# Kernel tuning notes

Measured on AMD Instinct MI355X. Metric: run time of the kernel, lower is better.

Reference implementation:

```python
import jax, jax.numpy as jnp
import numpy as np

N = 20000       # nodes per graph
E = 320000      # edges per graph (avg degree 16)
R = 8           # num_relations
B = 2           # batch of graphs
DIMS = [128, 256, 256, 128]  # in -> hidden -> hidden -> out
SLOPE = 0.2     # LeakyReLU negative slope


def setup_inputs() -> dict:
    key = jax.random.key(0)
    ks = jax.random.split(key, 12)
    inp = {
        "x": jax.random.normal(ks[0], (B, N, DIMS[0]), dtype=jnp.float32),
        "edge_index": jax.random.randint(ks[1], (B, 2, E), 0, N, dtype=jnp.int32),
        "edge_type": jax.random.randint(ks[2], (B, E), 0, R, dtype=jnp.int32),
    }
    for l in range(3):
        cin, cout = DIMS[l], DIMS[l + 1]
        s = 1.0 / np.sqrt(cin)
        inp[f"W{l}"] = jax.random.normal(ks[3 + 3 * l], (R, cin, cout), jnp.float32) * s
        inp[f"root{l}"] = jax.random.normal(ks[4 + 3 * l], (cin, cout), jnp.float32) * s
        inp[f"b{l}"] = jnp.zeros((cout,), jnp.float32)
    return inp


def _rgcn_layer(h, src, dst, etype, W, root, b):
    """One RGCNConv (per-relation mean aggregation) on a single graph.
    h: (N,Cin), src/dst/etype: (E,), W: (R,Cin,Cout), root: (Cin,Cout), b: (Cout,)
    """
    # transform every node by every relation weight once: (N,R,Cout)
    h_rel = jnp.einsum('nc,rcd->nrd', h, W)
    # per-edge message: gather source node transformed by that edge's relation
    msg = h_rel[src, etype]                               # (E,Cout)
    # per-(target-node, relation) mean, as in PyG's per-relation propagate
    seg = dst * R + etype                                 # (E,)
    sums = jax.ops.segment_sum(msg, seg, num_segments=N * R)
    cnt = jax.ops.segment_sum(jnp.ones((msg.shape[0],), h.dtype), seg,
                              num_segments=N * R)
    mean = sums / jnp.maximum(cnt, 1.0)[:, None]          # (N*R,Cout)
    agg = mean.reshape(N, R, -1).sum(axis=1)              # (N,Cout)
    return agg + h @ root + b


def reference(x, edge_index, edge_type, W0, root0, b0, W1, root1, b1, W2, root2, b2):
    params = [(W0, root0, b0), (W1, root1, b1), (W2, root2, b2)]

    def single(xg, ei, et):
        src, dst = ei[0], ei[1]
        h = xg
        for (W, root, b) in params:
            h = _rgcn_layer(h, src, dst, et, W, root, b)
            h = jnp.where(h > 0, h, SLOPE * h)  # LeakyReLU(0.2); dropout=identity (eval)
        return h

    return jax.vmap(single)(x, edge_index, edge_type)
```

## Files before the change

kernel.cpp:

```cpp
#include <hip/hip_runtime.h>
#include <hip/hip_bf16.h>

#define NN 20000
#define EE 320000
#define RR 8
#define NR (NN * RR)
#define NB 40
#define SCAP 640

typedef float f32x4 __attribute__((ext_vector_type(4)));
typedef float f32x2 __attribute__((ext_vector_type(2)));
typedef short s16x8 __attribute__((ext_vector_type(8)));

__device__ __forceinline__ unsigned short f2bf(float f) {
  unsigned u = __builtin_bit_cast(unsigned, f);
  unsigned r = u + 0x7FFFu + ((u >> 16) & 1u);
  return (unsigned short)(r >> 16);
}
__device__ __forceinline__ f32x2 bf2x2(unsigned u) {
  f32x2 r;
  r.x = __builtin_bit_cast(float, u << 16);
  r.y = __builtin_bit_cast(float, u & 0xFFFF0000u);
  return r;
}
__device__ __forceinline__ void gload_lds16(const void* g, void* l) {
  __builtin_amdgcn_global_load_lds(
      (const __attribute__((address_space(1))) unsigned*)g,
      (__attribute__((address_space(3))) unsigned*)l, 16, 0, 0);
}

__global__ void k_count(const int* __restrict__ ei, const int* __restrict__ et,
                        int* __restrict__ cnt) {
  int e = blockIdx.x * blockDim.x + threadIdx.x;
  int g = e >= EE;
  int el = e - g * EE;
  int d = ei[(size_t)g * 2 * EE + EE + el];
  int t = et[(size_t)g * EE + el];
  atomicAdd(&cnt[(size_t)g * NR + d * RR + t], 1);
}

__global__ __launch_bounds__(1024) void k_scan1(const int* __restrict__ cnt,
                                                int* __restrict__ off,
                                                int* __restrict__ btot) {
  int g = blockIdx.y, b = blockIdx.x;
  const int* c = cnt + (size_t)g * NR;
  int* o = off + (size_t)g * NR;
  __shared__ int wsum[16];
  int lane = threadIdx.x & 63, w = threadIdx.x >> 6;
  int i = b * 4096 + (int)threadIdx.x * 4;
  int4 v = {0, 0, 0, 0};
  if (i + 3 < NR) v = *(const int4*)&c[i];
  else {
    if (i < NR) v.x = c[i];
    if (i + 1 < NR) v.y = c[i + 1];
    if (i + 2 < NR) v.z = c[i + 2];
  }
  int s0 = v.x, s1 = s0 + v.y, s2 = s1 + v.z, s3 = s2 + v.w;
  int s = s3;
  for (int d = 1; d < 64; d <<= 1) {
    int t = __shfl_up(s, d);
    if (lane >= d) s += t;
  }
  if (lane == 63) wsum[w] = s;
  __syncthreads();
  if (threadIdx.x < 16) {
    int ws = wsum[threadIdx.x];
    for (int d = 1; d < 16; d <<= 1) {
      int t = __shfl_up(ws, d);
      if ((int)threadIdx.x >= d) ws += t;
    }
    wsum[threadIdx.x] = ws;
  }
  __syncthreads();
  int excl = (w > 0 ? wsum[w - 1] : 0) + (s - s3);
  if (i < NR) o[i] = excl;
  if (i + 1 < NR) o[i + 1] = excl + s0;
  if (i + 2 < NR) o[i + 2] = excl + s1;
  if (i + 3 < NR) o[i + 3] = excl + s2;
  if (threadIdx.x == 0) btot[g * NB + b] = wsum[15];
}

__global__ void k_scan2(const int* __restrict__ btot, int* __restrict__ bof) {
  int g = threadIdx.x >> 6, lane = threadIdx.x & 63;
  int v = (lane < NB) ? btot[g * NB + lane] : 0;
  int s = v;
  for (int d = 1; d < 64; d <<= 1) {
    int t = __shfl_up(s, d);
    if (lane >= d) s += t;
  }
  if (lane < NB) bof[g * NB + lane] = s - v;
}

__global__ __launch_bounds__(1024) void k_scan3(int* __restrict__ off,
                                                const int* __restrict__ bof) {
  int g = blockIdx.y;
  int add = bof[g * NB + blockIdx.x];
  int i = blockIdx.x * 4096 + (int)threadIdx.x * 4;
  int* o = off + (size_t)g * NR;
  if (i + 3 < NR) {
    int4 v = *(const int4*)&o[i];
    v.x += add; v.y += add; v.z += add; v.w += add;
    *(int4*)&o[i] = v;
  } else {
    for (int j = i; j < NR; ++j) o[j] += add;
  }
}

__global__ void k_scatter(const int* __restrict__ ei, const int* __restrict__ et,
                          int* __restrict__ off, int* __restrict__ ssrc) {
  int e = blockIdx.x * blockDim.x + threadIdx.x;
  int g = e >= EE;
  int el = e - g * EE;
  int s = ei[(size_t)g * 2 * EE + el];
  int d = ei[(size_t)g * 2 * EE + EE + el];
  int t = et[(size_t)g * EE + el];
  int pos = atomicAdd(&off[(size_t)g * NR + d * RR + t], 1);
  ssrc[(size_t)g * EE + pos] = s;
}

__global__ void k_cvt(const float* __restrict__ x, unsigned short* __restrict__ hX) {
  int i = (blockIdx.x * blockDim.x + threadIdx.x) * 4;
  if (i >= 2 * NN * 128) return;
  int g = i >= NN * 128;
  int il = i - g * NN * 128;
  float4 v = *(const float4*)&x[i];
  ushort4 o;
  o.x = f2bf(v.x); o.y = f2bf(v.y); o.z = f2bf(v.z); o.w = f2bf(v.w);
  *(ushort4*)&hX[(size_t)g * NN * 256 + il] = o;
}

__global__ void k_btf(const float* __restrict__ W, const float* __restrict__ root,
                      unsigned short* __restrict__ btf, int Cin, int Cout,
                      int Ktot) {
  int idx = blockIdx.x * blockDim.x + threadIdx.x;
  if (idx >= Cout * Ktot) return;
  int j = idx & 7;
  int lane = (idx >> 3) & 63;
  int kk = (idx >> 9) & 1;
  int t = idx >> 10;
  int fr = t % (Cout / 16);
  int s = t / (Cout / 16);
  int co = fr * 16 + (lane & 15);
  int k = s * 64 + kk * 32 + (lane >> 4) * 8 + j;
  int r = k / Cin, ci = k - r * Cin;
  float v = (r < RR) ? W[((size_t)r * Cin + ci) * Cout + co]
                     : root[(size_t)ci * Cout + co];
  btf[idx] = f2bf(v);
}

#define LOADB(bb, s)                                                           \
  _Pragma("unroll") for (int kk = 0; kk < 2; ++kk)                             \
      _Pragma("unroll") for (int f = 0; f < 4; ++f) bb[kk][f] =                \
          *(const s16x8*)(btl +                                                \
                          (size_t)(((s) * (COUT / 16) + wn16 + f) * 2 + kk) *  \
                              512);

#define MFMA_STEP_C(j, bb)                                                     \
  do {                                                                         \
    _Pragma("unroll") for (int kk = 0; kk < 2; ++kk) {                         \
      s16x8 a[MF];                                                             \
      _Pragma("unroll") for (int f = 0; f < MF; ++f) {                         \
        int row = wm + f * 16 + (lane & 15);                                   \
        int colb = kk * 64 + (lane >> 4) * 16;                                 \
        a[f] = *(const s16x8*)(As + (j)*ASTR + row * 128 +                     \
                               (colb ^ ((row & 7) << 4)));                     \
      }                                                                        \
      _Pragma("unroll") for (int fm = 0; fm < MF; ++fm)                        \
          _Pragma("unroll") for (int fn = 0; fn < 4; ++fn)                     \
              acc[fm][fn] = __builtin_amdgcn_mfma_f32_16x16x32_bf16(           \
                  a[fm], bb[kk][fn], acc[fm][fn], 0, 0, 0);                    \
    }                                                                          \
  } while (0)

#define ACC4(u)                                                                \
  {                                                                            \
    fa2[c][0] += bf2x2((u).x);                                                 \
    fa2[c][1] += bf2x2((u).y);                                                 \
    fa2[c][2] += bf2x2((u).z);                                                 \
    fa2[c][3] += bf2x2((u).w);                                                 \
  }

template <int CIN, int COUT, bool OUTF32>
__global__ __launch_bounds__(256) void k_fused(
    const int* __restrict__ ssrc, const int* __restrict__ off,
    const unsigned short* __restrict__ h, const unsigned short* __restrict__ btf,
    const float* __restrict__ bias, void* __restrict__ outp) {
  constexpr int KTOT = (RR + 1) * CIN;
  constexpr int NS = KTOT / 64;
  constexpr int CH = CIN / 64;
  constexpr int RPP = 8 / CH;
  constexpr int NPH = RR / RPP;
  constexpr int CPT = CIN / 8;
  constexpr int NCH = CPT / 8;
  constexpr int NWN = COUT / 64;
  constexpr int MW = 4 / NWN;
  constexpr int WR = 32 / MW;
  constexpr int MF = WR / 16;
  constexpr int ASTR = 4112;
  constexpr int SH = (CIN == 256) ? 9 : 8;
  static_assert(RPP * CH == 8, "phase holds 8 sub-tiles");
  __shared__ char As[8 * ASTR];
  __shared__ int offs[32][9];
  __shared__ int sseg[SCAP];
  const int tid = threadIdx.x, lane = tid & 63, wave = tid >> 6;
  const int wn = (wave % NWN) * 64;
  const int wn16 = wn >> 4;
  const int wm = (wave / NWN) * WR;
  const int m0 = blockIdx.x * 32;
  const int g = blockIdx.z;
  ssrc += (size_t)g * EE;
  off += (size_t)g * NR;
  h += (size_t)g * NN * 256;

  for (int idx = tid; idx < 32 * 9; idx += 256) {
    int row = idx / 9, j = idx - row * 9;
    int seg0 = (m0 + row) * RR;
    offs[row][j] = (j == 0) ? (seg0 == 0 ? 0 : off[seg0 - 1]) : off[seg0 + j - 1];
  }
  const int segA = m0 * RR;
  const int ebase = (segA == 0) ? 0 : off[segA - 1];
  const int eend = off[(m0 + 32) * RR - 1];
  const int cntE = eend - ebase;
  const bool inl = cntE <= SCAP;
  if (inl)
    for (int i = tid; i < cntE; i += 256) sseg[i] = ssrc[ebase + i] << SH;
  __syncthreads();

  f32x4 acc[MF][4] = {};
  const int arow = tid >> 3;
  const int q = tid & 7;
  const int swzA = (arow & 7) << 4;
  const char* hqB = (const char*)h + (size_t)q * CPT * 2;
  const unsigned short* btl = btf + lane * 8;

  auto produce = [&](int r) {
    f32x2 fa2[NCH][4];
#pragma unroll
    for (int c = 0; c < NCH; ++c)
#pragma unroll
      for (int w = 0; w < 4; ++w) fa2[c][w] = (f32x2)(0.f);
    const int o0 = offs[arow][r], o1 = offs[arow][r + 1];
    if (inl) {
      int e = o0 - ebase;
      const int e1 = o1 - ebase;
      for (; e + 1 < e1; e += 2) {
        const unsigned short* pa = (const unsigned short*)(hqB + sseg[e]);
        const unsigned short* pb = (const unsigned short*)(hqB + sseg[e + 1]);
#pragma unroll
        for (int c = 0; c < NCH; ++c) {
          uint4 ua = *(const uint4*)(pa + c * 8);
          uint4 ub = *(const uint4*)(pb + c * 8);
          ACC4(ua);
          ACC4(ub);
        }
      }
      if (e < e1) {
        const unsigned short* pa = (const unsigned short*)(hqB + sseg[e]);
#pragma unroll
        for (int c = 0; c < NCH; ++c) {
          uint4 ua = *(const uint4*)(pa + c * 8);
          ACC4(ua);
        }
      }
    } else {
      for (int e = o0; e < o1; ++e) {
        const unsigned short* pa = (const unsigned short*)(hqB + (ssrc[e] << SH));
#pragma unroll
        for (int c = 0; c < NCH; ++c) {
          uint4 ua = *(const uint4*)(pa + c * 8);
          ACC4(ua);
        }
      }
    }
    float inv = 1.0f / fmaxf((float)(o1 - o0), 1.0f);
    char* half = As + (r % RPP) * (CH * ASTR);
#pragma unroll
    for (int c = 0; c < NCH; ++c) {
      s16x8 mbv;
#pragma unroll
      for (int w = 0; w < 4; ++w) {
        mbv[2 * w] = (short)f2bf(fa2[c][w].x * inv);
        mbv[2 * w + 1] = (short)f2bf(fa2[c][w].y * inv);
      }
      int colb = (q * CPT + c * 8) * 2;
      int ct = colb >> 7;
      int wb = colb & 127;
      *(s16x8*)(half + ct * ASTR + arow * 128 + (wb ^ swzA)) = mbv;
    }
  };

  auto root_stage = [&]() {
#pragma unroll
    for (int i = 0; i < CH; ++i) {
      int o = i * ASTR + wave * 1024;
      int ob = wave * 1024 + lane * 16;
      int row = (ob >> 7) & 31;
      int wb = ob & 127;
      gload_lds16((const char*)h + ((size_t)(m0 + row) * CIN + i * 64) * 2 +
                      (wb ^ ((row & 7) << 4)),
                  As + o);
    }
  };

  s16x8 bc[2][4], bn[2][4];
  LOADB(bc, 0);
#pragma unroll
  for (int r0 = 0; r0 < RPP; ++r0) produce(r0);
  __syncthreads();

  for (int p = 0; p < NPH; ++p) {
#pragma unroll
    for (int j = 0; j < 8; j += 2) {
      int s = p * 8 + j;
      LOADB(bn, s + 1);
      __builtin_amdgcn_s_setprio(1);
      MFMA_STEP_C(j, bc);
      __builtin_amdgcn_s_setprio(0);
      LOADB(bc, s + 2);
      __builtin_amdgcn_s_setprio(1);
      MFMA_STEP_C(j + 1, bn);
      __builtin_amdgcn_s_setprio(0);
    }
    __syncthreads();
    if (p < NPH - 1) {
#pragma unroll
      for (int r0 = 0; r0 < RPP; ++r0) produce((p + 1) * RPP + r0);
    } else {
      root_stage();
    }
    __syncthreads();
  }
#pragma unroll
  for (int c = 0; c < CH; c += 2) {
    int s = RR * CH + c;
    if (s + 1 < NS) { LOADB(bn, s + 1); }
    __builtin_amdgcn_s_setprio(1);
    MFMA_STEP_C(c, bc);
    __builtin_amdgcn_s_setprio(0);
    if (s + 2 < NS) { LOADB(bc, s + 2); }
    __builtin_amdgcn_s_setprio(1);
    MFMA_STEP_C(c + 1, bn);
    __builtin_amdgcn_s_setprio(0);
  }

#pragma unroll
  for (int fm = 0; fm < MF; ++fm) {
    int rbase = m0 + wm + fm * 16 + (lane >> 4) * 4;
#pragma unroll
    for (int fn = 0; fn < 4; ++fn) {
      int col = wn + fn * 16 + (lane & 15);
      float bv = bias[col];
#pragma unroll
      for (int v = 0; v < 4; ++v) {
        int row = rbase + v;
        float xv = acc[fm][fn][v] + bv;
        xv = xv > 0.f ? xv : 0.2f * xv;
        if constexpr (OUTF32)
          ((float*)outp)[(size_t)g * NN * COUT + (size_t)row * COUT + col] = xv;
        else
          ((unsigned short*)outp)[(size_t)g * NN * 256 + (size_t)row * COUT +
                                  col] = f2bf(xv);
      }
    }
  }
}

extern "C" void kernel_launch(void* const* d_in, const int* in_sizes, int n_in,
                              void* d_out, int out_size, void* d_ws, size_t ws_size,
                              hipStream_t stream) {
  const float* x  = (const float*)d_in[0];
  const int* ei   = (const int*)d_in[1];
  const int* etp  = (const int*)d_in[2];
  const float* W0 = (const float*)d_in[3];
  const float* r0 = (const float*)d_in[4];
  const float* b0 = (const float*)d_in[5];
  const float* W1 = (const float*)d_in[6];
  const float* r1 = (const float*)d_in[7];
  const float* b1 = (const float*)d_in[8];
  const float* W2 = (const float*)d_in[9];
  const float* r2 = (const float*)d_in[10];
  const float* b2 = (const float*)d_in[11];

  char* p = (char*)d_ws;
  unsigned short* hX  = (unsigned short*)p; p += (size_t)2 * NN * 256 * 2;
  unsigned short* h_a = (unsigned short*)p; p += (size_t)2 * NN * 256 * 2;
  int* cnt  = (int*)p; p += (size_t)2 * NR * 4;
  int* off  = (int*)p; p += (size_t)2 * NR * 4;
  int* btot = (int*)p; p += (size_t)2 * NB * 4;
  int* bof  = (int*)p; p += (size_t)2 * NB * 4;
  int* ssrc = (int*)p; p += (size_t)2 * EE * 4;
  unsigned short* bt0 = (unsigned short*)p; p += (size_t)256 * 1152 * 2;
  unsigned short* bt1 = (unsigned short*)p; p += (size_t)256 * 2304 * 2;
  unsigned short* bt2 = (unsigned short*)p; p += (size_t)128 * 2304 * 2;

  k_btf<<<(256 * 1152 + 255) / 256, 256, 0, stream>>>(W0, r0, bt0, 128, 256, 1152);
  k_btf<<<(256 * 2304 + 255) / 256, 256, 0, stream>>>(W1, r1, bt1, 256, 256, 2304);
  k_btf<<<(128 * 2304 + 255) / 256, 256, 0, stream>>>(W2, r2, bt2, 256, 128, 2304);

  (void)hipMemsetAsync(cnt, 0, (size_t)2 * NR * 4, stream);
  k_count<<<2 * EE / 256, 256, 0, stream>>>(ei, etp, cnt);
  k_scan1<<<dim3(NB, 2), 1024, 0, stream>>>(cnt, off, btot);
  k_scan2<<<1, 128, 0, stream>>>(btot, bof);
  k_scan3<<<dim3(NB, 2), 1024, 0, stream>>>(off, bof);
  k_cvt<<<2 * NN * 128 / 4 / 256, 256, 0, stream>>>(x, hX);
  k_scatter<<<2 * EE / 256, 256, 0, stream>>>(ei, etp, off, ssrc);

  k_fused<128, 256, false><<<dim3(625, 1, 2), 256, 0, stream>>>(
      ssrc, off, hX, bt0, b0, h_a);
  k_fused<256, 256, false><<<dim3(625, 1, 2), 256, 0, stream>>>(
      ssrc, off, h_a, bt1, b1, hX);
  k_fused<256, 128, true><<<dim3(625, 1, 2), 256, 0, stream>>>(
      ssrc, off, hX, bt2, b2, d_out);
}
```

Baseline: 345.4 us.

## Split relation K-range across two blocks with fp32 staging and separate activation kernel

Each fused layer kernel now launches twice as many blocks, with each half handling four of the eight relations (the second half also does the root term). Partial fp32 accumulators go to a staging buffer, and a new elementwise kernel sums the two halves, adds bias and applies LeakyReLU. The aim is more parallelism and occupancy across the GPU, since the original grid had only 1250 blocks. In exchange it adds fp32 staging writes and reads plus three extra kernel launches, and the edge-segment setup is repeated in both halves.

```diff
diff --git a/kernel.cpp b/kernel.cpp
--- a/kernel.cpp
+++ b/kernel.cpp
@@ -148,6 +148,31 @@
   btf[idx] = f2bf(v);
 }
 
+template <int COUT, bool OUTF32>
+__global__ void k_act(const float* __restrict__ stg, const float* __restrict__ bias,
+                      void* __restrict__ outp) {
+  int i = (blockIdx.x * blockDim.x + threadIdx.x) * 4;
+  if (i >= 2 * NN * COUT) return;
+  int g = i >= NN * COUT;
+  int local = i - g * NN * COUT;
+  int col = local & (COUT - 1);
+  float4 a = *(const float4*)&stg[(size_t)g * NN * COUT + local];
+  float4 b = *(const float4*)&stg[(size_t)(2 + g) * NN * COUT + local];
+  float4 bv = *(const float4*)&bias[col];
+  float4 o;
+  o.x = a.x + b.x + bv.x; o.x = o.x > 0.f ? o.x : 0.2f * o.x;
+  o.y = a.y + b.y + bv.y; o.y = o.y > 0.f ? o.y : 0.2f * o.y;
+  o.z = a.z + b.z + bv.z; o.z = o.z > 0.f ? o.z : 0.2f * o.z;
+  o.w = a.w + b.w + bv.w; o.w = o.w > 0.f ? o.w : 0.2f * o.w;
+  if constexpr (OUTF32) {
+    *(float4*)&((float*)outp)[(size_t)g * NN * COUT + local] = o;
+  } else {
+    ushort4 u;
+    u.x = f2bf(o.x); u.y = f2bf(o.y); u.z = f2bf(o.z); u.w = f2bf(o.w);
+    *(ushort4*)&((unsigned short*)outp)[(size_t)g * NN * 256 + local] = u;
+  }
+}
+
 #define LOADB(bb, s)                                                           \
   _Pragma("unroll") for (int kk = 0; kk < 2; ++kk)                             \
       _Pragma("unroll") for (int f = 0; f < 4; ++f) bb[kk][f] =                \
@@ -180,16 +205,29 @@
     fa2[c][3] += bf2x2((u).w);                                                 \
   }
 
-template <int CIN, int COUT, bool OUTF32>
+#define MFMA_PHASE(s0)                                                         \
+  _Pragma("unroll") for (int j = 0; j < 8; j += 2) {                           \
+    int s = (s0) + j;                                                          \
+    LOADB(bn, s + 1);                                                          \
+    __builtin_amdgcn_s_setprio(1);                                             \
+    MFMA_STEP_C(j, bc);                                                        \
+    __builtin_amdgcn_s_setprio(0);                                             \
+    if (s + 2 < NS) { LOADB(bc, s + 2); }                                      \
+    __builtin_amdgcn_s_setprio(1);                                             \
+    MFMA_STEP_C(j + 1, bn);                                                    \
+    __builtin_amdgcn_s_setprio(0);                                             \
+  }
+
+template <int CIN, int COUT>
 __global__ __launch_bounds__(256) void k_fused(
     const int* __restrict__ ssrc, const int* __restrict__ off,
     const unsigned short* __restrict__ h, const unsigned short* __restrict__ btf,
-    const float* __restrict__ bias, void* __restrict__ outp) {
+    float* __restrict__ stg) {
   constexpr int KTOT = (RR + 1) * CIN;
   constexpr int NS = KTOT / 64;
   constexpr int CH = CIN / 64;
   constexpr int RPP = 8 / CH;
-  constexpr int NPH = RR / RPP;
+  constexpr int NPHH = 4 / RPP;
   constexpr int CPT = CIN / 8;
   constexpr int NCH = CPT / 8;
   constexpr int NWN = COUT / 64;
@@ -207,6 +245,7 @@
   const int wn16 = wn >> 4;
   const int wm = (wave / NWN) * WR;
   const int m0 = blockIdx.x * 32;
+  const int half = blockIdx.y;
   const int g = blockIdx.z;
   ssrc += (size_t)g * EE;
   off += (size_t)g * NR;
@@ -232,6 +271,7 @@
   const int swzA = (arow & 7) << 4;
   const char* hqB = (const char*)h + (size_t)q * CPT * 2;
   const unsigned short* btl = btf + lane * 8;
+  const int rbaseH = half * 4;
 
   auto produce = [&](int r) {
     f32x2 fa2[NCH][4];
@@ -273,7 +313,7 @@
       }
     }
     float inv = 1.0f / fmaxf((float)(o1 - o0), 1.0f);
-    char* half = As + (r % RPP) * (CH * ASTR);
+    char* hbase = As + (r % RPP) * (CH * ASTR);
 #pragma unroll
     for (int c = 0; c < NCH; ++c) {
       s16x8 mbv;
@@ -285,7 +325,7 @@
       int colb = (q * CPT + c * 8) * 2;
       int ct = colb >> 7;
       int wb = colb & 127;
-      *(s16x8*)(half + ct * ASTR + arow * 128 + (wb ^ swzA)) = mbv;
+      *(s16x8*)(hbase + ct * ASTR + arow * 128 + (wb ^ swzA)) = mbv;
     }
   };
 
@@ -303,63 +343,49 @@
   };
 
   s16x8 bc[2][4], bn[2][4];
-  LOADB(bc, 0);
-#pragma unroll
-  for (int r0 = 0; r0 < RPP; ++r0) produce(r0);
+  LOADB(bc, rbaseH * CH);
+#pragma unroll
+  for (int r0 = 0; r0 < RPP; ++r0) produce(rbaseH + r0);
   __syncthreads();
 
-  for (int p = 0; p < NPH; ++p) {
-#pragma unroll
-    for (int j = 0; j < 8; j += 2) {
-      int s = p * 8 + j;
-      LOADB(bn, s + 1);
+  for (int p = 0; p < NPHH; ++p) {
+    MFMA_PHASE(rbaseH * CH + p * 8);
+    if (p < NPHH - 1) {
+      __syncthreads();
+#pragma unroll
+      for (int r0 = 0; r0 < RPP; ++r0) produce(rbaseH + (p + 1) * RPP + r0);
+      __syncthreads();
+    }
+  }
+  if (half == 1) {
+    __syncthreads();
+    root_stage();
+    __syncthreads();
+#pragma unroll
+    for (int c = 0; c < CH; c += 2) {
+      int s = RR * CH + c;
+      if (s + 1 < NS) { LOADB(bn, s + 1); }
       __builtin_amdgcn_s_setprio(1);
-      MFMA_STEP_C(j, bc);
+      MFMA_STEP_C(c, bc);
       __builtin_amdgcn_s_setprio(0);
-      LOADB(bc, s + 2);
+      if (s + 2 < NS) { LOADB(bc, s + 2); }
       __builtin_amdgcn_s_setprio(1);
-      MFMA_STEP_C(j + 1, bn);
+      MFMA_STEP_C(c + 1, bn);
       __builtin_amdgcn_s_setprio(0);
     }
-    __syncthreads();
-    if (p < NPH - 1) {
-#pragma unroll
-      for (int r0 = 0; r0 < RPP; ++r0) produce((p + 1) * RPP + r0);
-    } else {
-      root_stage();
-    }
-    __syncthreads();
-  }
-#pragma unroll
-  for (int c = 0; c < CH; c += 2) {
-    int s = RR * CH + c;
-    if (s + 1 < NS) { LOADB(bn, s + 1); }
-    __builtin_amdgcn_s_setprio(1);
-    MFMA_STEP_C(c, bc);
-    __builtin_amdgcn_s_setprio(0);
-    if (s + 2 < NS) { LOADB(bc, s + 2); }
-    __builtin_amdgcn_s_setprio(1);
-    MFMA_STEP_C(c + 1, bn);
-    __builtin_amdgcn_s_setprio(0);
-  }
-
+  }
+
+  float* sP = stg + (size_t)(half * 2 + g) * NN * COUT;
 #pragma unroll
   for (int fm = 0; fm < MF; ++fm) {
     int rbase = m0 + wm + fm * 16 + (lane >> 4) * 4;
 #pragma unroll
     for (int fn = 0; fn < 4; ++fn) {
       int col = wn + fn * 16 + (lane & 15);
-      float bv = bias[col];
 #pragma unroll
       for (int v = 0; v < 4; ++v) {
         int row = rbase + v;
-        float xv = acc[fm][fn][v] + bv;
-        xv = xv > 0.f ? xv : 0.2f * xv;
-        if constexpr (OUTF32)
-          ((float*)outp)[(size_t)g * NN * COUT + (size_t)row * COUT + col] = xv;
-        else
-          ((unsigned short*)outp)[(size_t)g * NN * 256 + (size_t)row * COUT +
-                                  col] = f2bf(xv);
+        sP[(size_t)row * COUT + col] = acc[fm][fn][v];
       }
     }
   }
@@ -384,6 +410,7 @@
   char* p = (char*)d_ws;
   unsigned short* hX  = (unsigned short*)p; p += (size_t)2 * NN * 256 * 2;
   unsigned short* h_a = (unsigned short*)p; p += (size_t)2 * NN * 256 * 2;
+  float* stg = (float*)p; p += (size_t)4 * NN * 256 * 4;
   int* cnt  = (int*)p; p += (size_t)2 * NR * 4;
   int* off  = (int*)p; p += (size_t)2 * NR * 4;
   int* btot = (int*)p; p += (size_t)2 * NB * 4;
@@ -405,10 +432,10 @@
   k_cvt<<<2 * NN * 128 / 4 / 256, 256, 0, stream>>>(x, hX);
   k_scatter<<<2 * EE / 256, 256, 0, stream>>>(ei, etp, off, ssrc);
 
-  k_fused<128, 256, false><<<dim3(625, 1, 2), 256, 0, stream>>>(
-      ssrc, off, hX, bt0, b0, h_a);
-  k_fused<256, 256, false><<<dim3(625, 1, 2), 256, 0, stream>>>(
-      ssrc, off, h_a, bt1, b1, hX);
-  k_fused<256, 128, true><<<dim3(625, 1, 2), 256, 0, stream>>>(
-      ssrc, off, hX, bt2, b2, d_out);
-}
+  k_fused<128, 256><<<dim3(625, 2, 2), 256, 0, stream>>>(ssrc, off, hX, bt0, stg);
+  k_act<256, false><<<10000, 256, 0, stream>>>(stg, b0, h_a);
+  k_fused<256, 256><<<dim3(625, 2, 2), 256, 0, stream>>>(ssrc, off, h_a, bt1, stg);
+  k_act<256, false><<<10000, 256, 0, stream>>>(stg, b1, hX);
+  k_fused<256, 128><<<dim3(625, 2, 2), 256, 0, stream>>>(ssrc, off, hX, bt2, stg);
+  k_act<128, true><<<5000, 256, 0, stream>>>(stg, b2, d_out);
+}
```

New measurement: 384.6 us. 11.3% more time.
